# Optimization experiments

Hardware: AMD Instinct MI355X
Metric: run time of the kernel (lower is better)

The kernel has to match this reference:

```python
import jax, jax.numpy as jnp
import numpy as np

T, S, B = 512, 512, 8
D, H = 512, 8
HD = D // H
L = 8            # nlabels
F = 2048         # dim_feedforward
EPS = 1e-5


def _ln(x, s, b):
    m = x.mean(-1, keepdims=True)
    v = ((x - m) ** 2).mean(-1, keepdims=True)
    return (x - m) * jax.lax.rsqrt(v + EPS) * s + b


def setup_inputs() -> dict:
    key = jax.random.key(0)
    ks = jax.random.split(key, 20)
    p = lambda i, shape: jax.random.normal(ks[i], shape, jnp.float32) * 0.02
    z = lambda n: jnp.zeros((n,), jnp.float32)
    return {
        "tgt": jax.random.normal(ks[0], (T, B, D), jnp.float32),
        "edge_mask": jax.random.uniform(ks[1], (B, L, T, T), dtype=jnp.float32),
        "tgt_padding_mask": jnp.zeros((B, T, T), jnp.bool_),
        "memory": jax.random.normal(ks[2], (S, B, D), jnp.float32),
        # self-attn (GNN matrix relational attention)
        "sa_q_w": p(3, (D, D)), "sa_q_b": z(D),
        "sa_k_w": p(4, (D, D)), "sa_k_b": z(D),
        "sa_v_w": p(5, (D, D)), "sa_v_b": z(D),
        "sa_rel": p(6, (L, HD, HD)),
        "sa_out_w": p(7, (D, D)), "sa_out_b": z(D),
        # cross-attn (torch MultiheadAttention packed in_proj)
        "ca_in_w": p(8, (3 * D, D)), "ca_in_b": z(3 * D),
        "ca_out_w": p(9, (D, D)), "ca_out_b": z(D),
        # FFN
        "lin1_w": p(10, (F, D)), "lin1_b": z(F),
        "lin2_w": p(11, (D, F)), "lin2_b": z(D),
        # layernorms
        "ln1_s": jnp.ones((D,), jnp.float32), "ln1_b": z(D),
        "ln2_s": jnp.ones((D,), jnp.float32), "ln2_b": z(D),
        "ln3_s": jnp.ones((D,), jnp.float32), "ln3_b": z(D),
    }


def reference(tgt, edge_mask, tgt_padding_mask, memory,
              sa_q_w, sa_q_b, sa_k_w, sa_k_b, sa_v_w, sa_v_b, sa_rel,
              sa_out_w, sa_out_b, ca_in_w, ca_in_b, ca_out_w, ca_out_b,
              lin1_w, lin1_b, lin2_w, lin2_b,
              ln1_s, ln1_b, ln2_s, ln2_b, ln3_s, ln3_b):
    scale = 1.0 / np.sqrt(HD).astype(np.float32)

    # ---- edge-aware relational self-attention (dropout = eval/identity) ----
    x = tgt.transpose(1, 0, 2)                       # (B, T, D)
    def heads(y, n):                                 # (B, n, ., HD)
        return y.reshape(B, -1, H, HD).transpose(0, 2, 1, 3)
    q = heads(x @ sa_q_w.T + sa_q_b, T)
    k = heads(x @ sa_k_w.T + sa_k_b, T)
    v = heads(x @ sa_v_w.T + sa_v_b, T)

    scores = jnp.zeros((B, H, T, T), q.dtype)
    for l in range(L):                               # small fixed label set
        kl = jnp.einsum('bhtd,de->bhte', k, sa_rel[l])
        scores = scores + edge_mask[:, l][:, None] * jnp.einsum('bhid,bhjd->bhij', q, kl)
    scores = scores * scale
    scores = jnp.where(tgt_padding_mask[:, None], -1e9, scores)
    attn = jax.nn.softmax(scores, axis=-1)
    o = jnp.einsum('bhij,bhjd->bhid', attn, v).transpose(0, 2, 1, 3).reshape(B, T, D)
    tgt2 = (o @ sa_out_w.T + sa_out_b).transpose(1, 0, 2)   # (T, B, D)
    x1 = _ln(tgt + tgt2, ln1_s, ln1_b)

    # ---- standard cross-attention over encoder memory ----
    wq, wk, wv = ca_in_w[:D], ca_in_w[D:2 * D], ca_in_w[2 * D:]
    bq, bk, bv = ca_in_b[:D], ca_in_b[D:2 * D], ca_in_b[2 * D:]
    cq = heads((x1 @ wq.T + bq).transpose(1, 0, 2), T)       # (B,H,T,HD)
    ck = heads((memory @ wk.T + bk).transpose(1, 0, 2), S)   # (B,H,S,HD)
    cv = heads((memory @ wv.T + bv).transpose(1, 0, 2), S)
    cs = jnp.einsum('bhtd,bhsd->bhts', cq, ck) * scale
    ca = jax.nn.softmax(cs, axis=-1)
    co = jnp.einsum('bhts,bhsd->bhtd', ca, cv).transpose(0, 2, 1, 3).reshape(B, T, D)
    tgt2 = (co @ ca_out_w.T + ca_out_b).transpose(1, 0, 2)
    x2 = _ln(x1 + tgt2, ln2_s, ln2_b)

    # ---- FFN ----
    ffn = jax.nn.relu(x2 @ lin1_w.T + lin1_b) @ lin2_w.T + lin2_b
    return _ln(x2 + ffn, ln3_s, ln3_b)
```

## Files before the change

### kernel.cpp

```cpp
#include <hip/hip_runtime.h>

#define Tn 512
#define Sn 512
#define Bn 8
#define Dn 512
#define Hn 8
#define HDn 64
#define Ln 8
#define Fn 2048
#define SCALE 0.125f

typedef short short8 __attribute__((ext_vector_type(8)));
typedef float floatx4 __attribute__((ext_vector_type(4)));

__device__ __forceinline__ unsigned short f2b(float f) {
    unsigned int u = __float_as_uint(f);
    u += 0x7FFFu + ((u >> 16) & 1u);
    return (unsigned short)(u >> 16);
}

__global__ __launch_bounds__(256) void to_rows_bf16(const float* __restrict__ in,
                                                    unsigned short* __restrict__ out, int T_) {
    size_t n = (size_t)blockIdx.x * 256 + threadIdx.x;
    size_t total = (size_t)T_ * Bn * Dn;
    if (n >= total) return;
    int d = (int)(n & (Dn - 1));
    size_t rt = n >> 9;
    int t = (int)(rt % T_);
    int b = (int)(rt / T_);
    out[n] = f2b(in[((size_t)t * Bn + b) * Dn + d]);
}

__global__ __launch_bounds__(256) void conv_all(
    const float* __restrict__ qw, const float* __restrict__ kw, const float* __restrict__ vw,
    const float* __restrict__ sow, const float* __restrict__ ciw, const float* __restrict__ cow,
    const float* __restrict__ l1w, const float* __restrict__ l2w, const float* __restrict__ rel,
    const float* __restrict__ qbias, const float* __restrict__ kbias, const float* __restrict__ vbias,
    unsigned short* __restrict__ wall, float* __restrict__ bqkv) {
    const int Q = 1 << 18;
    const int total = 16 * Q + Ln * HDn * HDn;
    int i = blockIdx.x * 256 + threadIdx.x;
    if (i < total) {
        int seg = i >> 18, r = i & (Q - 1);
        float v;
        if (seg < 3)       v = (seg == 0 ? qw : (seg == 1 ? kw : vw))[r];
        else if (seg == 3) v = sow[r];
        else if (seg < 7)  v = ciw[(size_t)(seg - 4) * Q + r];
        else if (seg == 7) v = cow[r];
        else if (seg < 12) v = l1w[(size_t)(seg - 8) * Q + r];
        else if (seg < 16) v = l2w[(size_t)(seg - 12) * Q + r];
        else               v = rel[r];
        wall[i] = f2b(v);
    }
    int j = i - total;
    if (j >= 0 && j < 3 * Dn)
        bqkv[j] = (j < Dn ? qbias[j] : (j < 2 * Dn ? kbias[j - Dn] : vbias[j - 2 * Dn]));
}

__device__ __forceinline__ void c_scatter(
    floatx4 v, int gm, int gn, size_t coff, int ldc, float alpha, float bb,
    int mode, int relu, int Tp, void* Cv, void* Cv2, void* Cv3) {
    for (int r = 0; r < 4; ++r) {
        float val = v[r] * alpha + bb;
        if (relu) val = fmaxf(val, 0.0f);
        int m = gm + r;
        if (mode == 0) {
            ((float*)Cv)[coff + (size_t)m * ldc + gn] = val;
        } else if (mode == 1) {
            ((unsigned short*)Cv)[coff + (size_t)m * ldc + gn] = f2b(val);
        } else if (mode == 2) {
            int bq = m / Tp, t = m - bq * Tp;
            ((unsigned short*)Cv)[(((size_t)(bq * Hn + (gn >> 6)) * Tp + t) << 6) + (gn & 63)] = f2b(val);
        } else if (mode == 3) {
            int bq = m / Tp, t = m - bq * Tp;
            ((unsigned short*)Cv)[((size_t)(bq * Hn + (gn >> 6)) * 64 + (gn & 63)) * Tp + t] = f2b(val);
        } else if (mode == 4) {
            int sel = gn >> 9, g2 = gn & 511;
            int bq = m / Tp, t = m - bq * Tp;
            int hh = g2 >> 6, dd = g2 & 63;
            if (sel == 0)
                ((unsigned short*)Cv)[(((size_t)(bq * Hn + hh) * Tp + t) << 6) + dd] = f2b(val);
            else if (sel == 1)
                ((unsigned short*)Cv2)[(((size_t)(bq * Hn + hh) * Tp + t) << 6) + dd] = f2b(val);
            else
                ((unsigned short*)Cv3)[((size_t)(bq * Hn + hh) * 64 + dd) * Tp + t] = f2b(val);
        } else {
            int sel = gn >> 9, g2 = gn & 511;
            int bq = m / Tp, t = m - bq * Tp;
            int hh = g2 >> 6, dd = g2 & 63;
            if (sel == 0)
                ((unsigned short*)Cv)[(((size_t)(bq * Hn + hh) * Tp + t) << 6) + dd] = f2b(val);
            else
                ((unsigned short*)Cv2)[((size_t)(bq * Hn + hh) * 64 + dd) * Tp + t] = f2b(val);
        }
    }
}

__global__ __launch_bounds__(256) void gemm_bf16(
    const unsigned short* __restrict__ A, const unsigned short* __restrict__ W,
    const float* __restrict__ bias, void* __restrict__ Cv, void* __restrict__ Cv2,
    void* __restrict__ Cv3,
    int M, int N, int K, int lda, int ldw, int ldc,
    long sA1, long sA2, long sW1, long sW2, long sC1, long sC2, int zdiv,
    float alpha, int mode, int relu, int Tp) {
    int z = blockIdx.z;
    int z1 = z / zdiv, z2 = z - z1 * zdiv;
    const unsigned short* Ab = A + (size_t)z1 * sA1 + (size_t)z2 * sA2;
    const unsigned short* Wb = W + (size_t)z1 * sW1 + (size_t)z2 * sW2;
    size_t coff = (size_t)z1 * sC1 + (size_t)z2 * sC2;
    int tid = threadIdx.x;
    int lane = tid & 63, wave = tid >> 6;
    int wm = wave & 1, wn = wave >> 1;
    int l16 = lane & 15, quad = lane >> 4;
    int m0 = blockIdx.y * 64 + wm * 32;
    int n0 = blockIdx.x * 64 + wn * 32;

    floatx4 acc00 = {0,0,0,0}, acc01 = {0,0,0,0}, acc10 = {0,0,0,0}, acc11 = {0,0,0,0};
    const unsigned short* a0p = Ab + (size_t)(m0 + l16) * lda + quad * 8;
    const unsigned short* a1p = a0p + (size_t)16 * lda;
    const unsigned short* b0p = Wb + (size_t)(n0 + l16) * ldw + quad * 8;
    const unsigned short* b1p = b0p + (size_t)16 * ldw;

#pragma unroll 2
    for (int kk = 0; kk < K; kk += 32) {
        short8 a0 = *(const short8*)(a0p + kk);
        short8 a1 = *(const short8*)(a1p + kk);
        short8 b0 = *(const short8*)(b0p + kk);
        short8 b1 = *(const short8*)(b1p + kk);
        acc00 = __builtin_amdgcn_mfma_f32_16x16x32_bf16(a0, b0, acc00, 0, 0, 0);
        acc01 = __builtin_amdgcn_mfma_f32_16x16x32_bf16(a0, b1, acc01, 0, 0, 0);
        acc10 = __builtin_amdgcn_mfma_f32_16x16x32_bf16(a1, b0, acc10, 0, 0, 0);
        acc11 = __builtin_amdgcn_mfma_f32_16x16x32_bf16(a1, b1, acc11, 0, 0, 0);
    }
    floatx4 accs[2][2] = {{acc00, acc01}, {acc10, acc11}};
    for (int mt = 0; mt < 2; ++mt)
        for (int nt = 0; nt < 2; ++nt) {
            int gn = n0 + nt * 16 + l16;
            float bb = bias ? bias[gn] : 0.0f;
            c_scatter(accs[mt][nt], m0 + mt * 16 + quad * 4, gn, coff, ldc,
                      alpha, bb, mode, relu, Tp, Cv, Cv2, Cv3);
        }
}

template <int MT, int NT>
__global__ __launch_bounds__(256) void gemmT_bf16(
    const unsigned short* __restrict__ A, const unsigned short* __restrict__ W,
    const float* __restrict__ bias, void* __restrict__ Cv, void* __restrict__ Cv2,
    void* __restrict__ Cv3,
    int K, int lda, int ldw, int ldc,
    float alpha, int mode, int relu, int Tp) {
    int tid = threadIdx.x;
    int lane = tid & 63, wave = tid >> 6;
    int wm = wave & 1, wn = wave >> 1;
    int l16 = lane & 15, quad = lane >> 4;
    int m0 = blockIdx.y * (MT * 32) + wm * (MT * 16);
    int n0 = blockIdx.x * (NT * 32) + wn * (NT * 16);

    floatx4 acc[MT][NT] = {};
    const unsigned short* ap = A + (size_t)(m0 + l16) * lda + quad * 8;
    const unsigned short* bp = W + (size_t)(n0 + l16) * ldw + quad * 8;

    for (int kk = 0; kk < K; kk += 32) {
        short8 a[MT], b[NT];
#pragma unroll
        for (int mt = 0; mt < MT; ++mt)
            a[mt] = *(const short8*)(ap + (size_t)mt * 16 * lda + kk);
#pragma unroll
        for (int nt = 0; nt < NT; ++nt)
            b[nt] = *(const short8*)(bp + (size_t)nt * 16 * ldw + kk);
#pragma unroll
        for (int mt = 0; mt < MT; ++mt)
#pragma unroll
            for (int nt = 0; nt < NT; ++nt)
                acc[mt][nt] = __builtin_amdgcn_mfma_f32_16x16x32_bf16(a[mt], b[nt], acc[mt][nt], 0, 0, 0);
    }
    for (int mt = 0; mt < MT; ++mt)
        for (int nt = 0; nt < NT; ++nt) {
            int gn = n0 + nt * 16 + l16;
            float bb = bias ? bias[gn] : 0.0f;
            c_scatter(acc[mt][nt], m0 + mt * 16 + quad * 4, gn, 0, ldc,
                      alpha, bb, mode, relu, Tp, Cv, Cv2, Cv3);
        }
}

__global__ __launch_bounds__(512, 2) void relsoft_em(
    const unsigned short* __restrict__ uR,
    const unsigned short* __restrict__ kB,
    const float* __restrict__ em,
    const unsigned char* __restrict__ pad,
    unsigned short* __restrict__ P) {
    int id = blockIdx.x;
    int r5 = id & 31, q5 = id >> 5;
    int hp = r5 >> 3;
    int uu = q5 * 8 + (r5 & 7);
    int b = uu >> 5, it = uu & 31;
    int h0 = hp * 2;
    int tid = threadIdx.x;
    int wave = tid >> 6, lane = tid & 63;
    int l16 = lane & 15, quad = lane >> 4;
    int i = it * 16 + l16;

    __shared__ float emS[3 * 8 * 1024];
    __shared__ float uS[256 * 32];
    __shared__ float redm[2][8][16];
    __shared__ float reds[2][8][16];

    const float* emBase = em + ((size_t)b * Ln * Tn + (size_t)it * 16) * Tn;

    auto stageEM = [&](int sl, int buf) {
        const float* rowb = emBase + (size_t)sl * Tn * Tn;
        float* wb = emS + (size_t)(buf * 8 + wave) * 1024;
#pragma unroll
        for (int k = 0; k < 4; ++k) {
            int s = k * 64 + lane;
            int rr = s >> 4, sc = s & 15;
            const float* gp = rowb + (size_t)rr * Tn + (wave * 16 + (sc ^ rr)) * 4;
            __builtin_amdgcn_global_load_lds(
                (const __attribute__((address_space(1))) void*)gp,
                (__attribute__((address_space(3))) void*)(wb + k * 256), 16, 0, 0);
        }
    };

    unsigned int puf[4];
#pragma unroll
    for (int jc = 0; jc < 4; ++jc)
        puf[jc] = *(const unsigned int*)(pad + ((size_t)b * Tn + i) * Tn +
                                         wave * 64 + jc * 16 + quad * 4);
    short8 kf[2][4][2];
#pragma unroll
    for (int hh = 0; hh < 2; ++hh)
#pragma unroll
        for (int jc = 0; jc < 4; ++jc) {
            const unsigned short* kp = kB + ((size_t)(b * Hn + h0 + hh) * Tn +
                                             wave * 64 + jc * 16 + l16) * HDn + quad * 8;
            kf[hh][jc][0] = *(const short8*)(kp);
            kf[hh][jc][1] = *(const short8*)(kp + 32);
        }
    __builtin_amdgcn_sched_barrier(0);
    asm volatile("s_waitcnt vmcnt(0)");
    __builtin_amdgcn_sched_barrier(0);

#pragma unroll
    for (int k = 0; k < 4; ++k) {
        int s = k * 64 + lane;
        int rl = s >> 3, sc = s & 7;
        int row = wave * 32 + rl;
        int hh = row >> 7, rem = row & 127;
        int ll = rem >> 4, ii = rem & 15;
        const unsigned short* gp = uR + (((size_t)(b * Hn + h0 + hh) * Ln + ll) * Tn +
                                         it * 16 + ii) * HDn + (sc ^ (ii & 7)) * 8;
        __builtin_amdgcn_global_load_lds(
            (const __attribute__((address_space(1))) void*)gp,
            (__attribute__((address_space(3))) void*)(uS + (size_t)wave * 1024 + k * 256),
            16, 0, 0);
    }
    __builtin_amdgcn_sched_barrier(0);
    stageEM(0, 0);
    __builtin_amdgcn_sched_barrier(0);
    stageEM(1, 1);
    __builtin_amdgcn_sched_barrier(0);
    stageEM(2, 2);
    __builtin_amdgcn_sched_barrier(0);
    asm volatile("s_waitcnt vmcnt(12)");
    __builtin_amdgcn_sched_barrier(0);
    __builtin_amdgcn_s_barrier();

    floatx4 sacc[2][4] = {};
#pragma clang loop unroll(disable)
    for (int l = 0; l < Ln; ++l) {
        int buf = l % 3;
        if (l < 6)       { asm volatile("s_waitcnt vmcnt(8)"); }
        else if (l == 6) { asm volatile("s_waitcnt vmcnt(4)"); }
        else             { asm volatile("s_waitcnt vmcnt(0)"); }
        __builtin_amdgcn_sched_barrier(0);

        const float* rb = emS + (size_t)(buf * 8 + wave) * 1024;
        floatx4 emr[4];
#pragma unroll
        for (int jc = 0; jc < 4; ++jc) {
            int sc = (jc * 4 + quad) ^ l16;
            emr[jc] = *(const floatx4*)(rb + l16 * 64 + sc * 4);
        }
        const float* u0row = uS + (size_t)((0 * Ln + l) * 16 + l16) * 32;
        const float* u1row = uS + (size_t)((1 * Ln + l) * 16 + l16) * 32;
        int us0 = (quad ^ (l16 & 7)) * 4;
        int us1 = ((quad + 4) ^ (l16 & 7)) * 4;
        short8 u0a = *(const short8*)(u0row + us0);
        short8 u0b = *(const short8*)(u0row + us1);
        short8 u1a = *(const short8*)(u1row + us0);
        short8 u1b = *(const short8*)(u1row + us1);
        asm volatile("s_waitcnt lgkmcnt(0)");
        __builtin_amdgcn_sched_barrier(0);
        if (l + 3 < Ln) stageEM(l + 3, buf);
        __builtin_amdgcn_sched_barrier(0);

#pragma unroll
        for (int jc = 0; jc < 4; ++jc) {
            floatx4 g0 = {0, 0, 0, 0};
            g0 = __builtin_amdgcn_mfma_f32_16x16x32_bf16(kf[0][jc][0], u0a, g0, 0, 0, 0);
            g0 = __builtin_amdgcn_mfma_f32_16x16x32_bf16(kf[0][jc][1], u0b, g0, 0, 0, 0);
            sacc[0][jc] += emr[jc] * g0;
            floatx4 g1 = {0, 0, 0, 0};
            g1 = __builtin_amdgcn_mfma_f32_16x16x32_bf16(kf[1][jc][0], u1a, g1, 0, 0, 0);
            g1 = __builtin_amdgcn_mfma_f32_16x16x32_bf16(kf[1][jc][1], u1b, g1, 0, 0, 0);
            sacc[1][jc] += emr[jc] * g1;
        }
    }

#pragma unroll
    for (int hh = 0; hh < 2; ++hh) {
        float mx = -3.0e38f;
#pragma unroll
        for (int jc = 0; jc < 4; ++jc) {
            floatx4 v = sacc[hh][jc] * SCALE;
            unsigned int pu = puf[jc];
            if (pu) {
                if (pu & 0x000000FFu) v[0] = -1.0e9f;
                if (pu & 0x0000FF00u) v[1] = -1.0e9f;
                if (pu & 0x00FF0000u) v[2] = -1.0e9f;
                if (pu & 0xFF000000u) v[3] = -1.0e9f;
            }
            sacc[hh][jc] = v;
            mx = fmaxf(mx, fmaxf(fmaxf(v[0], v[1]), fmaxf(v[2], v[3])));
        }
        mx = fmaxf(mx, __shfl_xor(mx, 16, 64));
        mx = fmaxf(mx, __shfl_xor(mx, 32, 64));
        if (quad == 0) redm[hh][wave][l16] = mx;
    }
    __syncthreads();
#pragma unroll
    for (int hh = 0; hh < 2; ++hh) {
        float m = redm[hh][0][l16];
#pragma unroll
        for (int w = 1; w < 8; ++w) m = fmaxf(m, redm[hh][w][l16]);
        float sum = 0.0f;
#pragma unroll
        for (int jc = 0; jc < 4; ++jc) {
            floatx4 v = sacc[hh][jc];
            v[0] = __expf(v[0] - m); v[1] = __expf(v[1] - m);
            v[2] = __expf(v[2] - m); v[3] = __expf(v[3] - m);
            sacc[hh][jc] = v;
            sum += v[0] + v[1] + v[2] + v[3];
        }
        sum += __shfl_xor(sum, 16, 64);
        sum += __shfl_xor(sum, 32, 64);
        if (quad == 0) reds[hh][wave][l16] = sum;
    }
    __syncthreads();
#pragma unroll
    for (int hh = 0; hh < 2; ++hh) {
        float sum = 0.0f;
#pragma unroll
        for (int w = 0; w < 8; ++w) sum += reds[hh][w][l16];
        float inv = 1.0f / sum;
        unsigned short* prow = P + ((size_t)(b * Hn + h0 + hh) * Tn + i) * Tn;
#pragma unroll
        for (int jc = 0; jc < 4; ++jc) {
            floatx4 v = sacc[hh][jc];
            ushort4 o;
            o.x = f2b(v[0] * inv); o.y = f2b(v[1] * inv);
            o.z = f2b(v[2] * inv); o.w = f2b(v[3] * inv);
            *(ushort4*)(prow + wave * 64 + jc * 16 + quad * 4) = o;
        }
    }
}

__global__ __launch_bounds__(256) void relsoft_nc(
    const unsigned short* __restrict__ qB,
    const unsigned short* __restrict__ kB,
    unsigned short* __restrict__ P) {
    int id = blockIdx.x;
    int c = id & 7, h = (id >> 3) & 7, g = id >> 6;
    int u = g * 8 + c;
    int b = u >> 5, it = u & 31;
    int bh = b * Hn + h;
    int wave = threadIdx.x >> 6, lane = threadIdx.x & 63;
    int l16 = lane & 15, quad = lane >> 4;
    int i = it * 16 + l16;
    const int JC = Sn / 64;

    __shared__ float redm[4][16];
    __shared__ float reds[4][16];

    const unsigned short* kp0 = kB + (size_t)bh * Sn * HDn + (size_t)l16 * HDn + quad * 8;
    short8 kf[JC][2];
#pragma unroll
    for (int jc = 0; jc < JC; ++jc) {
        const unsigned short* kp = kp0 + (size_t)(wave * JC + jc) * 16 * HDn;
        kf[jc][0] = *(const short8*)(kp);
        kf[jc][1] = *(const short8*)(kp + 32);
    }
    const unsigned short* ub = qB + (size_t)bh * Tn * HDn + (size_t)i * HDn + quad * 8;
    short8 u0 = *(const short8*)(ub);
    short8 u1 = *(const short8*)(ub + 32);

    floatx4 sacc[JC];
    float mx = -3.0e38f;
#pragma unroll
    for (int jc = 0; jc < JC; ++jc) {
        floatx4 gacc = {0, 0, 0, 0};
        gacc = __builtin_amdgcn_mfma_f32_16x16x32_bf16(kf[jc][0], u0, gacc, 0, 0, 0);
        gacc = __builtin_amdgcn_mfma_f32_16x16x32_bf16(kf[jc][1], u1, gacc, 0, 0, 0);
        floatx4 v = gacc * SCALE;
        sacc[jc] = v;
        mx = fmaxf(mx, fmaxf(fmaxf(v[0], v[1]), fmaxf(v[2], v[3])));
    }
    mx = fmaxf(mx, __shfl_xor(mx, 16, 64));
    mx = fmaxf(mx, __shfl_xor(mx, 32, 64));
    if (quad == 0) redm[wave][l16] = mx;
    __syncthreads();
    mx = fmaxf(fmaxf(redm[0][l16], redm[1][l16]), fmaxf(redm[2][l16], redm[3][l16]));

    float sum = 0.0f;
#pragma unroll
    for (int jc = 0; jc < JC; ++jc) {
        floatx4 v = sacc[jc];
        v[0] = __expf(v[0] - mx); v[1] = __expf(v[1] - mx);
        v[2] = __expf(v[2] - mx); v[3] = __expf(v[3] - mx);
        sacc[jc] = v;
        sum += v[0] + v[1] + v[2] + v[3];
    }
    sum += __shfl_xor(sum, 16, 64);
    sum += __shfl_xor(sum, 32, 64);
    if (quad == 0) reds[wave][l16] = sum;
    __syncthreads();
    sum = (reds[0][l16] + reds[1][l16]) + (reds[2][l16] + reds[3][l16]);
    float inv = 1.0f / sum;

    unsigned short* prow = P + (size_t)bh * Tn * Sn + (size_t)i * Sn;
#pragma unroll
    for (int jc = 0; jc < JC; ++jc) {
        int jt = wave * JC + jc;
        floatx4 v = sacc[jc];
        ushort4 o;
        o.x = f2b(v[0] * inv); o.y = f2b(v[1] * inv);
        o.z = f2b(v[2] * inv); o.w = f2b(v[3] * inv);
        *(ushort4*)(prow + jt * 16 + quad * 4) = o;
    }
}

__global__ __launch_bounds__(256) void ln_kernel(
    const float* __restrict__ a, int a_trans, const float* __restrict__ b2,
    const float* __restrict__ s, const float* __restrict__ bb,
    float* __restrict__ outF, int out_trans, unsigned short* __restrict__ outB) {
    int row = blockIdx.x;
    int b = row >> 9, t = row & (Tn - 1);
    int tid = threadIdx.x;
    size_t ia = a_trans ? ((size_t)(t * Bn + b)) * Dn : (size_t)row * Dn;
    size_t ir = (size_t)row * Dn;
    float x0 = a[ia + tid];
    float x1 = a[ia + tid + 256];
    if (b2) { x0 += b2[ir + tid]; x1 += b2[ir + tid + 256]; }
    float s1 = x0 + x1, s2 = x0 * x0 + x1 * x1;
    for (int off = 32; off; off >>= 1) {
        s1 += __shfl_xor(s1, off, 64);
        s2 += __shfl_xor(s2, off, 64);
    }
    __shared__ float red[2][4];
    int wave = tid >> 6, lane = tid & 63;
    if (lane == 0) { red[0][wave] = s1; red[1][wave] = s2; }
    __syncthreads();
    float ts1 = red[0][0] + red[0][1] + red[0][2] + red[0][3];
    float ts2 = red[1][0] + red[1][1] + red[1][2] + red[1][3];
    float mean = ts1 * (1.0f / Dn);
    float var = ts2 * (1.0f / Dn) - mean * mean;
    float rs = rsqrtf(var + 1e-5f);
    float y0 = (x0 - mean) * rs * s[tid] + bb[tid];
    float y1 = (x1 - mean) * rs * s[tid + 256] + bb[tid + 256];
    size_t io = out_trans ? ((size_t)(t * Bn + b)) * Dn : ir;
    if (outF) { outF[io + tid] = y0; outF[io + tid + 256] = y1; }
    if (outB) { outB[ir + tid] = f2b(y0); outB[ir + tid + 256] = f2b(y1); }
}

extern "C" void kernel_launch(void* const* d_in, const int* in_sizes, int n_in,
                              void* d_out, int out_size, void* d_ws, size_t ws_size,
                              hipStream_t stream) {
    const float* tgt      = (const float*)d_in[0];
    const float* em       = (const float*)d_in[1];
    const unsigned char* pad = (const unsigned char*)d_in[2];
    const float* memr     = (const float*)d_in[3];
    const float* sa_q_w   = (const float*)d_in[4];
    const float* sa_q_b   = (const float*)d_in[5];
    const float* sa_k_w   = (const float*)d_in[6];
    const float* sa_k_b   = (const float*)d_in[7];
    const float* sa_v_w   = (const float*)d_in[8];
    const float* sa_v_b   = (const float*)d_in[9];
    const float* sa_rel   = (const float*)d_in[10];
    const float* sa_out_w = (const float*)d_in[11];
    const float* sa_out_b = (const float*)d_in[12];
    const float* ca_in_w  = (const float*)d_in[13];
    const float* ca_in_b  = (const float*)d_in[14];
    const float* ca_out_w = (const float*)d_in[15];
    const float* ca_out_b = (const float*)d_in[16];
    const float* lin1_w   = (const float*)d_in[17];
    const float* lin1_b   = (const float*)d_in[18];
    const float* lin2_w   = (const float*)d_in[19];
    const float* lin2_b   = (const float*)d_in[20];
    const float* ln1_s    = (const float*)d_in[21];
    const float* ln1_b    = (const float*)d_in[22];
    const float* ln2_s    = (const float*)d_in[23];
    const float* ln2_b    = (const float*)d_in[24];
    const float* ln3_s    = (const float*)d_in[25];
    const float* ln3_b    = (const float*)d_in[26];

    const size_t BT = (size_t)Bn * Tn;
    const size_t Q  = 1 << 18;

    char* ws = (char*)d_ws;
    size_t off = 0;
    auto alloc = [&](size_t bytes) -> char* {
        char* p = ws + off;
        off += (bytes + 255) & ~(size_t)255;
        return p;
    };
    unsigned short* xb   = (unsigned short*)alloc(BT * Dn * 2);
    unsigned short* mb   = (unsigned short*)alloc(BT * Dn * 2);
    unsigned short* wall = (unsigned short*)alloc((16 * Q + Ln * HDn * HDn) * 2);
    float*          bqkv = (float*)alloc(3 * Dn * 4);
    unsigned short* qb   = (unsigned short*)alloc(BT * Dn * 2);
    unsigned short* kb   = (unsigned short*)alloc(BT * Dn * 2);
    unsigned short* vtb  = (unsigned short*)alloc(BT * Dn * 2);
    unsigned short* ur   = (unsigned short*)alloc((size_t)Bn * Hn * Ln * Tn * HDn * 2);
    unsigned short* pb   = (unsigned short*)alloc((size_t)Bn * Hn * Tn * Tn * 2);
    unsigned short* ob   = (unsigned short*)alloc(BT * Dn * 2);
    float*          t2f  = (float*)alloc(BT * Dn * 4);
    float*          x1f  = (float*)alloc(BT * Dn * 4);
    unsigned short* x1b  = (unsigned short*)alloc(BT * Dn * 2);
    float*          x2f  = (float*)alloc(BT * Dn * 4);
    unsigned short* x2b  = (unsigned short*)alloc(BT * Dn * 2);
    unsigned short* hid  = (unsigned short*)alloc(BT * Fn * 2);
    (void)ws_size; (void)in_sizes; (void)n_in; (void)out_size;

    unsigned short* wqkv = wall;
    unsigned short* wsao = wall + 3 * Q;
    unsigned short* wcain = wall + 4 * Q;
    unsigned short* wcao = wall + 7 * Q;
    unsigned short* wlin1 = wall + 8 * Q;
    unsigned short* wlin2 = wall + 12 * Q;
    unsigned short* wrel = wall + 16 * Q;

    auto gemm = [&](const unsigned short* A, const unsigned short* W, const float* bias,
                    void* C, void* C2, void* C3, int M, int N, int K, int lda, int ldw, int ldc,
                    long sA1, long sA2, long sW1, long sW2, long sC1, long sC2,
                    int zdiv, int batches, float alpha, int mode, int relu, int Tp) {
        dim3 g(N / 64, M / 64, batches);
        gemm_bf16<<<g, 256, 0, stream>>>(A, W, bias, C, C2, C3, M, N, K, lda, ldw, ldc,
                                         sA1, sA2, sW1, sW2, sC1, sC2, zdiv,
                                         alpha, mode, relu, Tp);
    };
    auto gemmBig = [&](const unsigned short* A, const unsigned short* W, const float* bias,
                       void* C, void* C2, void* C3, int M, int N, int K,
                       int lda, int ldw, int ldc, float alpha, int mode, int relu, int Tp) {
        dim3 g(N / 128, M / 128, 1);
        gemmT_bf16<4, 4><<<g, 256, 0, stream>>>(A, W, bias, C, C2, C3, K, lda, ldw, ldc,
                                                alpha, mode, relu, Tp);
    };
    auto gemmMed = [&](const unsigned short* A, const unsigned short* W, const float* bias,
                       void* C, void* C2, void* C3, int M, int N, int K,
                       int lda, int ldw, int ldc, float alpha, int mode, int relu, int Tp) {
        dim3 g(N / 64, M / 128, 1);
        gemmT_bf16<4, 2><<<g, 256, 0, stream>>>(A, W, bias, C, C2, C3, K, lda, ldw, ldc,
                                                alpha, mode, relu, Tp);
    };

    to_rows_bf16<<<dim3((BT * Dn + 255) / 256), 256, 0, stream>>>(tgt, xb, Tn);
    to_rows_bf16<<<dim3((BT * Dn + 255) / 256), 256, 0, stream>>>(memr, mb, Sn);
    conv_all<<<dim3((16 * Q + Ln * HDn * HDn + 3 * Dn + 255) / 256), 256, 0, stream>>>(
        sa_q_w, sa_k_w, sa_v_w, sa_out_w, ca_in_w, ca_out_w, lin1_w, lin2_w, sa_rel,
        sa_q_b, sa_k_b, sa_v_b, wall, bqkv);

    gemmBig(xb, wqkv, bqkv, qb, kb, vtb, (int)BT, 3 * Dn, Dn, Dn, Dn, 0, 1.0f, 4, 0, Tn);
    gemm(qb, wrel, nullptr, ur, nullptr, nullptr, Tn, HDn, HDn, HDn, HDn, HDn,
         (long)Tn * HDn, 0, 0, (long)HDn * HDn, (long)Ln * Tn * HDn, (long)Tn * HDn,
         Ln, Bn * Hn * Ln, 1.0f, 1, 0, 0);
    relsoft_em<<<dim3(1024), 512, 0, stream>>>(ur, kb, em, pad, pb);
    gemm(pb, vtb, nullptr, ob, nullptr, nullptr, Tn, HDn, Tn, Tn, Tn, Dn,
         (long)Hn * Tn * Tn, (long)Tn * Tn, (long)Hn * HDn * Tn, (long)HDn * Tn,
         (long)Tn * Dn, 64, Hn, Bn * Hn, 1.0f, 1, 0, 0);
    gemmMed(ob, wsao, sa_out_b, t2f, nullptr, nullptr, (int)BT, Dn, Dn, Dn, Dn, Dn,
            1.0f, 0, 0, 0);
    ln_kernel<<<dim3((int)BT), 256, 0, stream>>>(tgt, 1, t2f, ln1_s, ln1_b, x1f, 0, x1b);

    gemmMed(x1b, wcain, ca_in_b, qb, nullptr, nullptr, (int)BT, Dn, Dn, Dn, Dn, 0,
            1.0f, 2, 0, Tn);
    gemmBig(mb, wcain + (size_t)Dn * Dn, ca_in_b + Dn, kb, vtb, nullptr, (int)BT, 2 * Dn, Dn,
            Dn, Dn, 0, 1.0f, 5, 0, Sn);
    relsoft_nc<<<dim3(2048), 256, 0, stream>>>(qb, kb, pb);
    gemm(pb, vtb, nullptr, ob, nullptr, nullptr, Tn, HDn, Sn, Sn, Sn, Dn,
         (long)Hn * Tn * Sn, (long)Tn * Sn, (long)Hn * HDn * Sn, (long)HDn * Sn,
         (long)Tn * Dn, 64, Hn, Bn * Hn, 1.0f, 1, 0, 0);
    gemmMed(ob, wcao, ca_out_b, t2f, nullptr, nullptr, (int)BT, Dn, Dn, Dn, Dn, Dn,
            1.0f, 0, 0, 0);
    ln_kernel<<<dim3((int)BT), 256, 0, stream>>>(x1f, 0, t2f, ln2_s, ln2_b, x2f, 0, x2b);

    gemmBig(x2b, wlin1, lin1_b, hid, nullptr, nullptr, (int)BT, Fn, Dn, Dn, Dn, Fn,
            1.0f, 1, 1, 0);
    gemmMed(hid, wlin2, lin2_b, t2f, nullptr, nullptr, (int)BT, Dn, Fn, Fn, Fn, Dn,
            1.0f, 0, 0, 0);
    ln_kernel<<<dim3((int)BT), 256, 0, stream>>>(x2f, 0, t2f, ln3_s, ln3_b, (float*)d_out, 1, nullptr);
}
```

Measured before the change: 615.6 us.

## Stage GEMM tiles in LDS via direct global-to-LDS loads with XOR swizzle

The bf16 GEMM kernel now loads each K-slice of the A and W tiles into shared memory cooperatively, using global_load_lds with an XOR swizzle to avoid bank conflicts. Waves then read MFMA fragments from LDS instead of each wave loading its own operands straight from global memory. This is meant to cut redundant global traffic across waves. The cost is two barriers per 32-wide K step with no double buffering, which exposes load latency.

```diff
diff --git a/kernel.cpp b/kernel.cpp
--- a/kernel.cpp
+++ b/kernel.cpp
@@ -149,31 +149,63 @@
     void* __restrict__ Cv3,
     int K, int lda, int ldw, int ldc,
     float alpha, int mode, int relu, int Tp) {
+    const int RA = MT * 32, RB = NT * 32;
+    __shared__ unsigned short As[RA * 32];
+    __shared__ unsigned short Bs[RB * 32];
+
     int tid = threadIdx.x;
     int lane = tid & 63, wave = tid >> 6;
     int wm = wave & 1, wn = wave >> 1;
     int l16 = lane & 15, quad = lane >> 4;
-    int m0 = blockIdx.y * (MT * 32) + wm * (MT * 16);
-    int n0 = blockIdx.x * (NT * 32) + wn * (NT * 16);
+    int bm0 = blockIdx.y * RA;
+    int bn0 = blockIdx.x * RB;
 
     floatx4 acc[MT][NT] = {};
-    const unsigned short* ap = A + (size_t)(m0 + l16) * lda + quad * 8;
-    const unsigned short* bp = W + (size_t)(n0 + l16) * ldw + quad * 8;
 
     for (int kk = 0; kk < K; kk += 32) {
+        __syncthreads();
+#pragma unroll
+        for (int q = wave; q < RA / 16; q += 4) {
+            int idx = q * 64 + lane;
+            int m = idx >> 2, g = idx & 3;
+            const unsigned short* gp = A + (size_t)(bm0 + m) * lda + kk + ((g ^ (m & 3)) << 3);
+            __builtin_amdgcn_global_load_lds(
+                (const __attribute__((address_space(1))) void*)gp,
+                (__attribute__((address_space(3))) void*)(As + q * 512), 16, 0, 0);
+        }
+#pragma unroll
+        for (int q = wave; q < RB / 16; q += 4) {
+            int idx = q * 64 + lane;
+            int n = idx >> 2, g = idx & 3;
+            const unsigned short* gp = W + (size_t)(bn0 + n) * ldw + kk + ((g ^ (n & 3)) << 3);
+            __builtin_amdgcn_global_load_lds(
+                (const __attribute__((address_space(1))) void*)gp,
+                (__attribute__((address_space(3))) void*)(Bs + q * 512), 16, 0, 0);
+        }
+        __syncthreads();
+
         short8 a[MT], b[NT];
 #pragma unroll
-        for (int mt = 0; mt < MT; ++mt)
-            a[mt] = *(const short8*)(ap + (size_t)mt * 16 * lda + kk);
-#pragma unroll
-        for (int nt = 0; nt < NT; ++nt)
-            b[nt] = *(const short8*)(bp + (size_t)nt * 16 * ldw + kk);
+        for (int mt = 0; mt < MT; ++mt) {
+            int m = wm * (MT * 16) + mt * 16 + l16;
+            int g = quad ^ (m & 3);
+            a[mt] = *(const short8*)(As + m * 32 + g * 8);
+        }
+#pragma unroll
+        for (int nt = 0; nt < NT; ++nt) {
+            int n = wn * (NT * 16) + nt * 16 + l16;
+            int g = quad ^ (n & 3);
+            b[nt] = *(const short8*)(Bs + n * 32 + g * 8);
+        }
 #pragma unroll
         for (int mt = 0; mt < MT; ++mt)
 #pragma unroll
             for (int nt = 0; nt < NT; ++nt)
                 acc[mt][nt] = __builtin_amdgcn_mfma_f32_16x16x32_bf16(a[mt], b[nt], acc[mt][nt], 0, 0, 0);
     }
+
+    int m0 = bm0 + wm * (MT * 16);
+    int n0 = bn0 + wn * (NT * 16);
     for (int mt = 0; mt < MT; ++mt)
         for (int nt = 0; nt < NT; ++nt) {
             int gn = n0 + nt * 16 + l16;
```

New measurement: 880.2 us. 43.0% more time.

## Stage GEMM tiles through padded shared memory with register prefetch

Applied to the files above, without the earlier changes.

The templated bf16 GEMM now loads each block's A and W tiles cooperatively into LDS, using a row stride padded to 40 elements, instead of having every wave read its fragments directly from global memory. The next k-slice is prefetched into registers while the current slice is consumed. The aim is to cut redundant global loads across waves and overlap memory latency with MFMA work. In exchange it adds two block barriers per k-step plus extra LDS traffic and register pressure.

```diff
diff --git a/kernel.cpp b/kernel.cpp
--- a/kernel.cpp
+++ b/kernel.cpp
@@ -149,31 +149,81 @@
     void* __restrict__ Cv3,
     int K, int lda, int ldw, int ldc,
     float alpha, int mode, int relu, int Tp) {
+    const int RA = MT * 32, RB = NT * 32;
+    const int LS = 40;
+    const int AG = (RA * 4) / 256;
+    const int BG = (RB * 4) / 256;
+    __shared__ unsigned short As[RA * LS];
+    __shared__ unsigned short Bs[RB * LS];
+
     int tid = threadIdx.x;
     int lane = tid & 63, wave = tid >> 6;
     int wm = wave & 1, wn = wave >> 1;
     int l16 = lane & 15, quad = lane >> 4;
-    int m0 = blockIdx.y * (MT * 32) + wm * (MT * 16);
-    int n0 = blockIdx.x * (NT * 32) + wn * (NT * 16);
+    int bm0 = blockIdx.y * RA;
+    int bn0 = blockIdx.x * RB;
 
     floatx4 acc[MT][NT] = {};
-    const unsigned short* ap = A + (size_t)(m0 + l16) * lda + quad * 8;
-    const unsigned short* bp = W + (size_t)(n0 + l16) * ldw + quad * 8;
+    short8 av[AG], bv[BG];
+
+#pragma unroll
+    for (int g = 0; g < AG; ++g) {
+        int gi = g * 256 + tid;
+        int row = gi >> 2, cg = gi & 3;
+        av[g] = *(const short8*)(A + (size_t)(bm0 + row) * lda + cg * 8);
+    }
+#pragma unroll
+    for (int g = 0; g < BG; ++g) {
+        int gi = g * 256 + tid;
+        int row = gi >> 2, cg = gi & 3;
+        bv[g] = *(const short8*)(W + (size_t)(bn0 + row) * ldw + cg * 8);
+    }
 
     for (int kk = 0; kk < K; kk += 32) {
+        __syncthreads();
+#pragma unroll
+        for (int g = 0; g < AG; ++g) {
+            int gi = g * 256 + tid;
+            int row = gi >> 2, cg = gi & 3;
+            *(short8*)(As + row * LS + cg * 8) = av[g];
+        }
+#pragma unroll
+        for (int g = 0; g < BG; ++g) {
+            int gi = g * 256 + tid;
+            int row = gi >> 2, cg = gi & 3;
+            *(short8*)(Bs + row * LS + cg * 8) = bv[g];
+        }
+        __syncthreads();
+        if (kk + 32 < K) {
+#pragma unroll
+            for (int g = 0; g < AG; ++g) {
+                int gi = g * 256 + tid;
+                int row = gi >> 2, cg = gi & 3;
+                av[g] = *(const short8*)(A + (size_t)(bm0 + row) * lda + kk + 32 + cg * 8);
+            }
+#pragma unroll
+            for (int g = 0; g < BG; ++g) {
+                int gi = g * 256 + tid;
+                int row = gi >> 2, cg = gi & 3;
+                bv[g] = *(const short8*)(W + (size_t)(bn0 + row) * ldw + kk + 32 + cg * 8);
+            }
+        }
         short8 a[MT], b[NT];
 #pragma unroll
         for (int mt = 0; mt < MT; ++mt)
-            a[mt] = *(const short8*)(ap + (size_t)mt * 16 * lda + kk);
+            a[mt] = *(const short8*)(As + (wm * (MT * 16) + mt * 16 + l16) * LS + quad * 8);
 #pragma unroll
         for (int nt = 0; nt < NT; ++nt)
-            b[nt] = *(const short8*)(bp + (size_t)nt * 16 * ldw + kk);
+            b[nt] = *(const short8*)(Bs + (wn * (NT * 16) + nt * 16 + l16) * LS + quad * 8);
 #pragma unroll
         for (int mt = 0; mt < MT; ++mt)
 #pragma unroll
             for (int nt = 0; nt < NT; ++nt)
                 acc[mt][nt] = __builtin_amdgcn_mfma_f32_16x16x32_bf16(a[mt], b[nt], acc[mt][nt], 0, 0, 0);
     }
+
+    int m0 = bm0 + wm * (MT * 16);
+    int n0 = bn0 + wn * (NT * 16);
     for (int mt = 0; mt < MT; ++mt)
         for (int nt = 0; nt < NT; ++nt) {
             int gn = n0 + nt * 16 + l16;
```

New measurement: 832.3 us. 35.2% more time.
